# Optimization experiments

Hardware: AMD Instinct MI355X
Metric: run time of the kernel (lower is better)

The kernel has to match this reference:

```python
import jax, jax.numpy as jnp
import numpy as np

B, CIN, H, W = 8, 512, 32, 32
NH = 8
DQ = DK = DV = 256  # int(0.5 * Cin)
COUT = 512


def setup_inputs() -> dict:
    key = jax.random.key(0)
    k0, k1, k2, k3, k4 = jax.random.split(key, 5)
    x = jax.random.normal(k0, (B, CIN, H, W), dtype=jnp.float32)
    # 1x1 conv weights stored as [out, in] matrices (kernel size 1)
    w_qkv = jax.random.normal(k1, (DQ + DK + DV, CIN), dtype=jnp.float32) * 0.02
    b_qkv = jax.random.normal(k2, (DQ + DK + DV,), dtype=jnp.float32) * 0.02
    w_attn = jax.random.normal(k3, (COUT, DV), dtype=jnp.float32) * 0.02
    b_attn = jax.random.normal(k4, (COUT,), dtype=jnp.float32) * 0.02
    return {"x": x, "w_qkv": w_qkv, "b_qkv": b_qkv, "w_attn": w_attn, "b_attn": b_attn}


def _split_heads(t):
    b, c, h, w = t.shape
    return t.reshape(b, NH, c // NH, h, w)


def reference(x, w_qkv, b_qkv, w_attn, b_attn):
    b, _, h, w = x.shape
    hw = h * w
    # 1x1 conv == per-pixel GEMM
    qkv = jnp.einsum('bchw,oc->bohw', x, w_qkv) + b_qkv[None, :, None, None]
    q = qkv[:, :DQ]
    k = qkv[:, DQ:DQ + DK]
    v = qkv[:, DQ + DK:]
    dkh = DK // NH
    q = _split_heads(q) * (dkh ** -0.5)
    k = _split_heads(k)
    v = _split_heads(v)
    flat_q = q.reshape(b, NH, DQ // NH, hw)
    flat_k = k.reshape(b, NH, DK // NH, hw)
    flat_v = v.reshape(b, NH, DV // NH, hw)
    # logits: [b, NH, hw, hw]  (q^T k over feature dim)
    logits = jnp.einsum('bndq,bndk->bnqk', flat_q, flat_k)
    # FAITHFUL quirk: softmax over the HEAD axis (dim=1), as in the source
    weights = jax.nn.softmax(logits, axis=1)
    # attn_out: [b, NH, hw, dvh]
    attn_out = jnp.einsum('bnqk,bndk->bnqd', weights, flat_v)
    # FAITHFUL quirk: raw reshape (no transpose) to [b, NH, dvh, H, W]
    attn_out = attn_out.reshape(b, NH, DV // NH, h, w).reshape(b, DV, h, w)
    out = jnp.einsum('bchw,oc->bohw', attn_out, w_attn) + b_attn[None, :, None, None]
    return out
```

## Files before the change

### kernel.cpp

```cpp
#include <hip/hip_runtime.h>
#include <math.h>

#define BATCH 8
#define CIN   512
#define DQKV  768
#define NHEAD 8
#define HW    1024

typedef __attribute__((ext_vector_type(8))) short  short8;
typedef __attribute__((ext_vector_type(4))) float  float4v;

__device__ __forceinline__ ushort f2bf(float f) {
    union { float f; unsigned u; } c; c.f = f;
    unsigned u = c.u + 0x7fffu + ((c.u >> 16) & 1u);
    return (ushort)(u >> 16);
}

__device__ __forceinline__ void async_ld16(const ushort* g, ushort* l) {
    auto gp = (const __attribute__((address_space(1))) unsigned int*)g;
    auto lp = (__attribute__((address_space(3))) unsigned int*)l;
    __builtin_amdgcn_global_load_lds(gp, lp, 16, 0, 0);
}

__global__ __launch_bounds__(256)
void transpose_cvt(const float* __restrict__ in, ushort* __restrict__ out,
                   int K, int N)
{
    __shared__ float Ts[64][65];
    const int b  = blockIdx.z;
    const int k0 = blockIdx.y * 64;
    const int n0 = blockIdx.x * 64;
    const int t  = threadIdx.x;
    const float* ib = in + (size_t)b * K * N;
    ushort*      ob = out + (size_t)b * N * K;

    const int r  = t >> 4;
    const int c4 = (t & 15) * 4;
    #pragma unroll
    for (int p = 0; p < 4; ++p) {
        float4 v = *(const float4*)(ib + (size_t)(k0 + r + 16 * p) * N + n0 + c4);
        Ts[r + 16 * p][c4 + 0] = v.x;
        Ts[r + 16 * p][c4 + 1] = v.y;
        Ts[r + 16 * p][c4 + 2] = v.z;
        Ts[r + 16 * p][c4 + 3] = v.w;
    }
    __syncthreads();

    const int nl = t >> 3;
    const int kc = (t & 7) * 8;
    #pragma unroll
    for (int p = 0; p < 2; ++p) {
        int n = nl + 32 * p;
        uint4 u;
        u.x = (uint)f2bf(Ts[kc + 0][n]) | ((uint)f2bf(Ts[kc + 1][n]) << 16);
        u.y = (uint)f2bf(Ts[kc + 2][n]) | ((uint)f2bf(Ts[kc + 3][n]) << 16);
        u.z = (uint)f2bf(Ts[kc + 4][n]) | ((uint)f2bf(Ts[kc + 5][n]) << 16);
        u.w = (uint)f2bf(Ts[kc + 6][n]) | ((uint)f2bf(Ts[kc + 7][n]) << 16);
        *(uint4*)(ob + (size_t)(n0 + n) * K + k0 + kc) = u;
    }
}

__global__ void cvt_bf16(const float* __restrict__ in, ushort* __restrict__ out, int n8)
{
    int i = blockIdx.x * blockDim.x + threadIdx.x;
    if (i >= n8) return;
    const float4* p = (const float4*)(in + (size_t)i * 8);
    float4 a = p[0], b = p[1];
    uint4 u;
    u.x = (uint)f2bf(a.x) | ((uint)f2bf(a.y) << 16);
    u.y = (uint)f2bf(a.z) | ((uint)f2bf(a.w) << 16);
    u.z = (uint)f2bf(b.x) | ((uint)f2bf(b.y) << 16);
    u.w = (uint)f2bf(b.z) | ((uint)f2bf(b.w) << 16);
    *(uint4*)(out + (size_t)i * 8) = u;
}

__global__ __launch_bounds__(256)
void qk_transform(const ushort* __restrict__ qkv, ushort* __restrict__ Qt,
                  ushort* __restrict__ Kt)
{
    __shared__ ushort Ts[32 * 264];
    const int b   = blockIdx.z;
    const int g   = blockIdx.y;
    const int sp0 = blockIdx.x * 256;
    const int t   = threadIdx.x;

    const ushort* src = qkv + ((size_t)b * DQKV + g * 32) * HW;
    ushort* dst = (g < 8 ? Qt : Kt) + ((size_t)b * NHEAD + (g & 7)) * (HW * 32);

    #pragma unroll
    for (int p = 0; p < 4; ++p) {
        int d = (t >> 5) + p * 8;
        int c = t & 31;
        uint4 u = *(const uint4*)(src + (size_t)d * HW + sp0 + c * 8);
        *(uint4*)&Ts[d * 264 + c * 8] = u;
    }
    __syncthreads();

    ushort* orow = dst + (size_t)(sp0 + t) * 32;
    #pragma unroll
    for (int c = 0; c < 4; ++c) {
        ushort v[8];
        #pragma unroll
        for (int j = 0; j < 8; ++j) v[j] = Ts[(c * 8 + j) * 264 + t];
        *(uint4*)(orow + c * 8) = *(uint4*)v;
    }
}

template<int M, int K, bool QSCALE, bool OUTBF>
__global__ __launch_bounds__(256, 2)
void gemm_bt(const ushort* __restrict__ A, const ushort* __restrict__ Bt,
             const float* __restrict__ bias, void* __restrict__ Oo)
{
    __shared__ __align__(16) ushort As[128 * 64];
    __shared__ __align__(16) ushort Bs[128 * 64];

    const int b    = blockIdx.z;
    const int m0   = blockIdx.y * 128;
    const int n0   = blockIdx.x * 128;
    const int t    = threadIdx.x;
    const int lane = t & 63;
    const int wave = t >> 6;
    const int l16  = lane & 15;
    const int quad = lane >> 4;
    const int wm   = (wave & 1) * 64;
    const int wn   = (wave >> 1) * 64;

    const ushort* Bb = Bt + (size_t)b * HW * K;

    float4v acc[4][4];
    #pragma unroll
    for (int i = 0; i < 4; ++i)
        #pragma unroll
        for (int j = 0; j < 4; ++j)
            acc[i][j] = (float4v){0.f, 0.f, 0.f, 0.f};

    const int srow = t >> 3;
    const int sg   = t & 7;

    for (int k0 = 0; k0 < K; k0 += 64) {
        __syncthreads();
        #pragma unroll
        for (int is = 0; is < 4; ++is) {
            int row = srow + is * 32;
            int gch = sg ^ (row & 7);
            async_ld16(A  + (size_t)(m0 + row) * K + k0 + gch * 8,
                       As + (size_t)t * 8 + is * 2048);
            async_ld16(Bb + (size_t)(n0 + row) * K + k0 + gch * 8,
                       Bs + (size_t)t * 8 + is * 2048);
        }
        __syncthreads();

        #pragma unroll
        for (int ks = 0; ks < 2; ++ks) {
            short8 af[4], bf[4];
            #pragma unroll
            for (int i = 0; i < 4; ++i) {
                int row = wm + i * 16 + l16;
                int ch  = (ks * 4 + quad) ^ (row & 7);
                af[i] = *(const short8*)&As[row * 64 + ch * 8];
            }
            #pragma unroll
            for (int j = 0; j < 4; ++j) {
                int row = wn + j * 16 + l16;
                int ch  = (ks * 4 + quad) ^ (row & 7);
                bf[j] = *(const short8*)&Bs[row * 64 + ch * 8];
            }
            #pragma unroll
            for (int i = 0; i < 4; ++i)
                #pragma unroll
                for (int j = 0; j < 4; ++j)
                    acc[i][j] = __builtin_amdgcn_mfma_f32_16x16x32_bf16(
                        af[i], bf[j], acc[i][j], 0, 0, 0);
        }
    }

    #pragma unroll
    for (int i = 0; i < 4; ++i) {
        #pragma unroll
        for (int rr = 0; rr < 4; ++rr) {
            int m = m0 + wm + i * 16 + quad * 4 + rr;
            float bi = bias[m];
            float sc = QSCALE ? ((m < 256) ? 0.17677669529663687f : 1.0f) : 1.0f;
            #pragma unroll
            for (int j = 0; j < 4; ++j) {
                int n = n0 + wn + j * 16 + l16;
                float val = (acc[i][j][rr] + bi) * sc;
                if (OUTBF)
                    ((ushort*)Oo)[((size_t)b * M + m) * HW + n] = f2bf(val);
                else
                    ((float*)Oo)[((size_t)b * M + m) * HW + n] = val;
            }
        }
    }
}

__global__ __launch_bounds__(256, 2)
void attn_kernel(const ushort* __restrict__ qkv, const ushort* __restrict__ Qt,
                 const ushort* __restrict__ Kt, ushort* __restrict__ ab)
{
    __shared__ __align__(16) ushort Qs[NHEAD * 16 * 40];
    __shared__ __align__(16) ushort Ks[NHEAD * 32 * 40];
    __shared__ __align__(16) ushort Vs[NHEAD * 32 * 40];
    __shared__ __align__(16) ushort Ws[NHEAD * 16 * 40];
    __shared__ float  Ss[NHEAD * 529];

    const int t    = threadIdx.x;
    const int b    = blockIdx.y;
    const int q0   = blockIdx.x * 16;
    const int wave = t >> 6;
    const int lane = t & 63;
    const int l16  = lane & 15;
    const int quad = lane >> 4;

    const ushort* qk  = qkv + (size_t)b * DQKV * HW;
    const ushort* Qtb = Qt + (size_t)b * NHEAD * HW * 32;
    const ushort* Ktb = Kt + (size_t)b * NHEAD * HW * 32;

    #pragma unroll
    for (int p = 0; p < 2; ++p) {
        int idx = t + p * 256;
        int n = idx >> 6, q = (idx >> 2) & 15, c = idx & 3;
        uint4 u = *(const uint4*)(Qtb + (size_t)n * (HW * 32) + (size_t)(q0 + q) * 32 + c * 8);
        *(uint4*)&Qs[(n * 16 + q) * 40 + c * 8] = u;
    }

    float4v acc[2][2];
    #pragma unroll
    for (int i = 0; i < 2; ++i)
        #pragma unroll
        for (int j = 0; j < 2; ++j)
            acc[i][j] = (float4v){0.f, 0.f, 0.f, 0.f};

    const int sq = t >> 4;
    const int sk = (t & 15) * 2;

    for (int k0 = 0; k0 < HW; k0 += 32) {
        __syncthreads();

        #pragma unroll
        for (int p = 0; p < 4; ++p) {
            int idx = t + p * 256;
            int n = idx >> 7, r = (idx >> 2) & 31, c = idx & 3;
            uint4 ku = *(const uint4*)(Ktb + (size_t)n * (HW * 32) + (size_t)(k0 + r) * 32 + c * 8);
            *(uint4*)&Ks[(n * 32 + r) * 40 + c * 8] = ku;
            uint4 vu = *(const uint4*)(qk + (size_t)(512 + n * 32 + r) * HW + k0 + c * 8);
            *(uint4*)&Vs[(n * 32 + r) * 40 + c * 8] = vu;
        }
        __syncthreads();

        #pragma unroll
        for (int hh = 0; hh < 2; ++hh) {
            int h = wave * 2 + hh;
            short8 a = *(const short8*)&Qs[(h * 16 + l16) * 40 + quad * 8];
            #pragma unroll
            for (int ko = 0; ko < 2; ++ko) {
                short8 bfr = *(const short8*)&Ks[(h * 32 + ko * 16 + l16) * 40 + quad * 8];
                float4v s = __builtin_amdgcn_mfma_f32_16x16x32_bf16(
                    a, bfr, (float4v){0.f, 0.f, 0.f, 0.f}, 0, 0, 0);
                float* sp = &Ss[h * 529 + (quad * 4) * 33 + ko * 16 + l16];
                #pragma unroll
                for (int r = 0; r < 4; ++r) sp[r * 33] = s[r];
            }
        }
        __syncthreads();

        {
            float v[NHEAD][2];
            float m0v = -1e30f, m1v = -1e30f;
            #pragma unroll
            for (int n = 0; n < NHEAD; ++n) {
                v[n][0] = Ss[n * 529 + sq * 33 + sk + 0];
                v[n][1] = Ss[n * 529 + sq * 33 + sk + 1];
                m0v = fmaxf(m0v, v[n][0]);
                m1v = fmaxf(m1v, v[n][1]);
            }
            float s0 = 0.f, s1 = 0.f;
            #pragma unroll
            for (int n = 0; n < NHEAD; ++n) {
                v[n][0] = __expf(v[n][0] - m0v);
                v[n][1] = __expf(v[n][1] - m1v);
                s0 += v[n][0];
                s1 += v[n][1];
            }
            float i0 = 1.0f / s0, i1 = 1.0f / s1;
            #pragma unroll
            for (int n = 0; n < NHEAD; ++n) {
                uint pk = (uint)f2bf(v[n][0] * i0) | ((uint)f2bf(v[n][1] * i1) << 16);
                *(uint*)&Ws[(n * 16 + sq) * 40 + sk] = pk;
            }
        }
        __syncthreads();

        #pragma unroll
        for (int hh = 0; hh < 2; ++hh) {
            int h = wave * 2 + hh;
            short8 a = *(const short8*)&Ws[(h * 16 + l16) * 40 + quad * 8];
            #pragma unroll
            for (int dd = 0; dd < 2; ++dd) {
                short8 bfr = *(const short8*)&Vs[(h * 32 + dd * 16 + l16) * 40 + quad * 8];
                acc[hh][dd] = __builtin_amdgcn_mfma_f32_16x16x32_bf16(
                    a, bfr, acc[hh][dd], 0, 0, 0);
            }
        }
    }

    #pragma unroll
    for (int hh = 0; hh < 2; ++hh) {
        int h = wave * 2 + hh;
        #pragma unroll
        for (int dd = 0; dd < 2; ++dd) {
            int d = dd * 16 + l16;
            #pragma unroll
            for (int r = 0; r < 4; ++r) {
                int qg = q0 + quad * 4 + r;
                size_t addr = ((size_t)b * HW + (size_t)((qg & 31) * 32 + d)) * 256
                            + h * 32 + (qg >> 5);
                ab[addr] = f2bf(acc[hh][dd][r]);
            }
        }
    }
}

extern "C" void kernel_launch(void* const* d_in, const int* in_sizes, int n_in,
                              void* d_out, int out_size, void* d_ws, size_t ws_size,
                              hipStream_t stream)
{
    const float* x      = (const float*)d_in[0];
    const float* w_qkv  = (const float*)d_in[1];
    const float* b_qkv  = (const float*)d_in[2];
    const float* w_attn = (const float*)d_in[3];
    const float* b_attn = (const float*)d_in[4];
    float* out = (float*)d_out;

    ushort* qkv_b = (ushort*)d_ws;
    ushort* xb    = qkv_b + 6291456;
    ushort* Qt    = xb;
    ushort* Kt    = xb + 2097152;
    ushort* ab    = xb + 4194304;
    ushort* wb1   = ab + 2097152;
    ushort* wb2   = wb1 + 393216;

    cvt_bf16<<<192, 256, 0, stream>>>(w_qkv, wb1, 49152);
    cvt_bf16<<<64, 256, 0, stream>>>(w_attn, wb2, 16384);
    transpose_cvt<<<dim3(16, 8, BATCH), 256, 0, stream>>>(x, xb, CIN, HW);

    gemm_bt<DQKV, CIN, true, true>
        <<<dim3(8, 6, BATCH), 256, 0, stream>>>(wb1, xb, b_qkv, qkv_b);

    qk_transform<<<dim3(4, 16, BATCH), 256, 0, stream>>>(qkv_b, Qt, Kt);

    attn_kernel<<<dim3(HW / 16, BATCH), 256, 0, stream>>>(qkv_b, Qt, Kt, ab);

    gemm_bt<512, 256, false, false>
        <<<dim3(8, 4, BATCH), 256, 0, stream>>>(wb2, ab, b_attn, out);
}
```

Before: 178.2 us.

## Restructure attention kernel: register-resident Q, in-register head softmax, direct K/V loads

Rewrites the attention kernel so each 512-thread block handles 32 queries. Q fragments stay in registers for all heads, and each wave computes logits for a 16-key slice across all 8 heads. The cross-head softmax then runs entirely in registers, with no LDS round-trip for scores. Only the normalized weights go through LDS (one buffer, two barriers per 128 keys), while K and V fragments are read straight from global memory. This removes the K/V/S staging buffers and cuts barriers per key chunk, at the cost of more register pressure and uncoalesced, uncached-in-LDS global reads of K and V.

```diff
diff --git a/kernel.cpp b/kernel.cpp
--- a/kernel.cpp
+++ b/kernel.cpp
@@ -194,131 +194,123 @@
     }
 }
 
-__global__ __launch_bounds__(256, 2)
+#define WROW 136
+
+__global__ __launch_bounds__(512, 2)
 void attn_kernel(const ushort* __restrict__ qkv, const ushort* __restrict__ Qt,
                  const ushort* __restrict__ Kt, ushort* __restrict__ ab)
 {
-    __shared__ __align__(16) ushort Qs[NHEAD * 16 * 40];
-    __shared__ __align__(16) ushort Ks[NHEAD * 32 * 40];
-    __shared__ __align__(16) ushort Vs[NHEAD * 32 * 40];
-    __shared__ __align__(16) ushort Ws[NHEAD * 16 * 40];
-    __shared__ float  Ss[NHEAD * 529];
+    __shared__ __align__(16) ushort Ws[NHEAD * 32 * WROW];
 
     const int t    = threadIdx.x;
     const int b    = blockIdx.y;
-    const int q0   = blockIdx.x * 16;
+    const int q0   = blockIdx.x * 32;
     const int wave = t >> 6;
     const int lane = t & 63;
     const int l16  = lane & 15;
     const int quad = lane >> 4;
 
-    const ushort* qk  = qkv + (size_t)b * DQKV * HW;
-    const ushort* Qtb = Qt + (size_t)b * NHEAD * HW * 32;
-    const ushort* Ktb = Kt + (size_t)b * NHEAD * HW * 32;
-
-    #pragma unroll
-    for (int p = 0; p < 2; ++p) {
-        int idx = t + p * 256;
-        int n = idx >> 6, q = (idx >> 2) & 15, c = idx & 3;
-        uint4 u = *(const uint4*)(Qtb + (size_t)n * (HW * 32) + (size_t)(q0 + q) * 32 + c * 8);
-        *(uint4*)&Qs[(n * 16 + q) * 40 + c * 8] = u;
-    }
-
-    float4v acc[2][2];
+    const ushort* Vb  = qkv + ((size_t)b * DQKV + 512) * HW;
+    const ushort* Qtb = Qt + (size_t)b * (NHEAD * HW * 32);
+    const ushort* Ktb = Kt + (size_t)b * (NHEAD * HW * 32);
+
+    short8 qf[NHEAD][2];
+    #pragma unroll
+    for (int h = 0; h < NHEAD; ++h)
+        #pragma unroll
+        for (int qs = 0; qs < 2; ++qs)
+            qf[h][qs] = *(const short8*)(Qtb + ((size_t)h * HW + q0 + qs * 16 + l16) * 32 + quad * 8);
+
+    float4v oacc[2][2];
     #pragma unroll
     for (int i = 0; i < 2; ++i)
         #pragma unroll
         for (int j = 0; j < 2; ++j)
-            acc[i][j] = (float4v){0.f, 0.f, 0.f, 0.f};
-
-    const int sq = t >> 4;
-    const int sk = (t & 15) * 2;
-
-    for (int k0 = 0; k0 < HW; k0 += 32) {
+            oacc[i][j] = (float4v){0.f, 0.f, 0.f, 0.f};
+
+    for (int k0 = 0; k0 < HW; k0 += 128) {
+        const int kk = k0 + wave * 16 + l16;
+        float4v S[2][NHEAD];
+        #pragma unroll
+        for (int h = 0; h < NHEAD; ++h) {
+            short8 kf = *(const short8*)(Ktb + ((size_t)h * HW + kk) * 32 + quad * 8);
+            S[0][h] = __builtin_amdgcn_mfma_f32_16x16x32_bf16(
+                kf, qf[h][0], (float4v){0.f, 0.f, 0.f, 0.f}, 0, 0, 0);
+            S[1][h] = __builtin_amdgcn_mfma_f32_16x16x32_bf16(
+                kf, qf[h][1], (float4v){0.f, 0.f, 0.f, 0.f}, 0, 0, 0);
+        }
+
+        uint2 wpk[2][NHEAD];
+        #pragma unroll
+        for (int qs = 0; qs < 2; ++qs) {
+            float4v mx = S[qs][0];
+            #pragma unroll
+            for (int h = 1; h < NHEAD; ++h)
+                #pragma unroll
+                for (int r = 0; r < 4; ++r) mx[r] = fmaxf(mx[r], S[qs][h][r]);
+            float e[NHEAD][4];
+            float4v sum = (float4v){0.f, 0.f, 0.f, 0.f};
+            #pragma unroll
+            for (int h = 0; h < NHEAD; ++h)
+                #pragma unroll
+                for (int r = 0; r < 4; ++r) {
+                    e[h][r] = __expf(S[qs][h][r] - mx[r]);
+                    sum[r] += e[h][r];
+                }
+            float4v inv;
+            #pragma unroll
+            for (int r = 0; r < 4; ++r) inv[r] = __builtin_amdgcn_rcpf(sum[r]);
+            #pragma unroll
+            for (int h = 0; h < NHEAD; ++h) {
+                uint2 pk;
+                pk.x = (uint)f2bf(e[h][0] * inv[0]) | ((uint)f2bf(e[h][1] * inv[1]) << 16);
+                pk.y = (uint)f2bf(e[h][2] * inv[2]) | ((uint)f2bf(e[h][3] * inv[3]) << 16);
+                wpk[qs][h] = pk;
+            }
+        }
+
         __syncthreads();
 
         #pragma unroll
-        for (int p = 0; p < 4; ++p) {
-            int idx = t + p * 256;
-            int n = idx >> 7, r = (idx >> 2) & 31, c = idx & 3;
-            uint4 ku = *(const uint4*)(Ktb + (size_t)n * (HW * 32) + (size_t)(k0 + r) * 32 + c * 8);
-            *(uint4*)&Ks[(n * 32 + r) * 40 + c * 8] = ku;
-            uint4 vu = *(const uint4*)(qk + (size_t)(512 + n * 32 + r) * HW + k0 + c * 8);
-            *(uint4*)&Vs[(n * 32 + r) * 40 + c * 8] = vu;
-        }
+        for (int qs = 0; qs < 2; ++qs)
+            #pragma unroll
+            for (int h = 0; h < NHEAD; ++h)
+                *(uint2*)&Ws[(size_t)(h * 32 + qs * 16 + l16) * WROW + wave * 16 + quad * 4]
+                    = wpk[qs][h];
+
         __syncthreads();
 
         #pragma unroll
-        for (int hh = 0; hh < 2; ++hh) {
-            int h = wave * 2 + hh;
-            short8 a = *(const short8*)&Qs[(h * 16 + l16) * 40 + quad * 8];
-            #pragma unroll
-            for (int ko = 0; ko < 2; ++ko) {
-                short8 bfr = *(const short8*)&Ks[(h * 32 + ko * 16 + l16) * 40 + quad * 8];
-                float4v s = __builtin_amdgcn_mfma_f32_16x16x32_bf16(
-                    a, bfr, (float4v){0.f, 0.f, 0.f, 0.f}, 0, 0, 0);
-                float* sp = &Ss[h * 529 + (quad * 4) * 33 + ko * 16 + l16];
+        for (int ks = 0; ks < 4; ++ks) {
+            short8 wf[2], vf[2];
+            #pragma unroll
+            for (int qs = 0; qs < 2; ++qs)
+                wf[qs] = *(const short8*)&Ws[(size_t)(wave * 32 + qs * 16 + l16) * WROW + ks * 32 + quad * 8];
+            #pragma unroll
+            for (int ds = 0; ds < 2; ++ds)
+                vf[ds] = *(const short8*)(Vb + (size_t)(wave * 32 + ds * 16 + l16) * HW + k0 + ks * 32 + quad * 8);
+            #pragma unroll
+            for (int qs = 0; qs < 2; ++qs)
                 #pragma unroll
-                for (int r = 0; r < 4; ++r) sp[r * 33] = s[r];
-            }
-        }
-        __syncthreads();
-
-        {
-            float v[NHEAD][2];
-            float m0v = -1e30f, m1v = -1e30f;
-            #pragma unroll
-            for (int n = 0; n < NHEAD; ++n) {
-                v[n][0] = Ss[n * 529 + sq * 33 + sk + 0];
-                v[n][1] = Ss[n * 529 + sq * 33 + sk + 1];
-                m0v = fmaxf(m0v, v[n][0]);
-                m1v = fmaxf(m1v, v[n][1]);
-            }
-            float s0 = 0.f, s1 = 0.f;
-            #pragma unroll
-            for (int n = 0; n < NHEAD; ++n) {
-                v[n][0] = __expf(v[n][0] - m0v);
-                v[n][1] = __expf(v[n][1] - m1v);
-                s0 += v[n][0];
-                s1 += v[n][1];
-            }
-            float i0 = 1.0f / s0, i1 = 1.0f / s1;
-            #pragma unroll
-            for (int n = 0; n < NHEAD; ++n) {
-                uint pk = (uint)f2bf(v[n][0] * i0) | ((uint)f2bf(v[n][1] * i1) << 16);
-                *(uint*)&Ws[(n * 16 + sq) * 40 + sk] = pk;
-            }
-        }
-        __syncthreads();
-
-        #pragma unroll
-        for (int hh = 0; hh < 2; ++hh) {
-            int h = wave * 2 + hh;
-            short8 a = *(const short8*)&Ws[(h * 16 + l16) * 40 + quad * 8];
-            #pragma unroll
-            for (int dd = 0; dd < 2; ++dd) {
-                short8 bfr = *(const short8*)&Vs[(h * 32 + dd * 16 + l16) * 40 + quad * 8];
-                acc[hh][dd] = __builtin_amdgcn_mfma_f32_16x16x32_bf16(
-                    a, bfr, acc[hh][dd], 0, 0, 0);
-            }
-        }
-    }
-
-    #pragma unroll
-    for (int hh = 0; hh < 2; ++hh) {
-        int h = wave * 2 + hh;
-        #pragma unroll
-        for (int dd = 0; dd < 2; ++dd) {
-            int d = dd * 16 + l16;
+                for (int ds = 0; ds < 2; ++ds)
+                    oacc[qs][ds] = __builtin_amdgcn_mfma_f32_16x16x32_bf16(
+                        wf[qs], vf[ds], oacc[qs][ds], 0, 0, 0);
+        }
+    }
+
+    #pragma unroll
+    for (int qs = 0; qs < 2; ++qs)
+        #pragma unroll
+        for (int ds = 0; ds < 2; ++ds) {
+            int d = ds * 16 + l16;
             #pragma unroll
             for (int r = 0; r < 4; ++r) {
-                int qg = q0 + quad * 4 + r;
+                int qg = q0 + qs * 16 + quad * 4 + r;
                 size_t addr = ((size_t)b * HW + (size_t)((qg & 31) * 32 + d)) * 256
-                            + h * 32 + (qg >> 5);
-                ab[addr] = f2bf(acc[hh][dd][r]);
-            }
-        }
-    }
+                            + wave * 32 + (qg >> 5);
+                ab[addr] = f2bf(oacc[qs][ds][r]);
+            }
+        }
 }
 
 extern "C" void kernel_launch(void* const* d_in, const int* in_sizes, int n_in,
@@ -349,7 +341,7 @@
 
     qk_transform<<<dim3(4, 16, BATCH), 256, 0, stream>>>(qkv_b, Qt, Kt);
 
-    attn_kernel<<<dim3(HW / 16, BATCH), 256, 0, stream>>>(qkv_b, Qt, Kt, ab);
+    attn_kernel<<<dim3(HW / 32, BATCH), 512, 0, stream>>>(qkv_b, Qt, Kt, ab);
 
     gemm_bt<512, 256, false, false>
         <<<dim3(8, 4, BATCH), 256, 0, stream>>>(wb2, ab, b_attn, out);
```

Result: faster. 162.9 us (-8.6%).
